# Kernel optimization log

Hardware: AMD Instinct MI355X
Metric: run time of the kernel (lower is better)

Reference implementation:

```python
import jax, jax.numpy as jnp
import numpy as np

NUM_HEADS = 16
ROPE_THETA = 10000.0


def apply_rope(x, positions):
    # x: [B, H, S, D], positions: [S] int
    d = x.shape[-1]
    inv_freq = ROPE_THETA ** (-jnp.arange(0, d, 2, dtype=jnp.float32) / d)  # [D/2]
    ang = positions.astype(jnp.float32)[:, None] * inv_freq[None, :]        # [S, D/2]
    cos, sin = jnp.cos(ang), jnp.sin(ang)                                   # [S, D/2]
    x1, x2 = x[..., 0::2], x[..., 1::2]                                     # even/odd pairs
    r1 = x1 * cos - x2 * sin
    r2 = x1 * sin + x2 * cos
    return jnp.stack([r1, r2], axis=-1).reshape(x.shape)


def setup_inputs() -> dict:
    key = jax.random.key(0)
    k1, k2, k3 = jax.random.split(key, 3)
    B, S, D = 2, 2048, 2048
    x = jax.random.normal(k1, (B, S, D), dtype=jnp.float32)
    token_positions = jnp.arange(S, dtype=jnp.int64)
    w_qkv = jax.random.normal(k2, (D, 3 * D), dtype=jnp.float32) * (D ** -0.5)
    w_o = jax.random.normal(k3, (D, D), dtype=jnp.float32) * (D ** -0.5)
    return {"x": x, "token_positions": token_positions, "w_qkv": w_qkv, "w_o": w_o}


def reference(x, token_positions, w_qkv, w_o):
    B, S, D = x.shape
    H = NUM_HEADS
    hd = D // H
    qkv = x @ w_qkv                                   # [B, S, 3D]
    qkv = qkv.reshape(B, S, 3, H, hd)                 # split '(r h d)'
    q = jnp.transpose(qkv[:, :, 0], (0, 2, 1, 3))     # [B, H, S, hd]
    k = jnp.transpose(qkv[:, :, 1], (0, 2, 1, 3))
    v = jnp.transpose(qkv[:, :, 2], (0, 2, 1, 3))
    q = apply_rope(q, token_positions)
    k = apply_rope(k, token_positions)
    scale = 1.0 / jnp.sqrt(jnp.float32(hd))
    scores = jnp.einsum('bhqd,bhkd->bhqk', q, k) * scale  # [B, H, S, S]
    causal = jnp.tril(jnp.ones((S, S), dtype=bool))
    scores = jnp.where(causal[None, None], scores, jnp.float32(-1e30))
    attn = jax.nn.softmax(scores, axis=-1)
    a = jnp.einsum('bhqk,bhkd->bhqd', attn, v)            # [B, H, S, hd]
    a = jnp.transpose(a, (0, 2, 1, 3)).reshape(B, S, D)   # merge heads, h-major
    return a @ w_o
```

## Files before the change

kernel.cpp:

```cpp
#include <hip/hip_runtime.h>

#define SEQ  2048
#define DIM  2048
#define NH   16
#define HD   128
#define TDIM 6144
#define TT   4096

typedef float  f32x4  __attribute__((ext_vector_type(4)));
typedef __bf16 bf16x8 __attribute__((ext_vector_type(8)));

__device__ __forceinline__ unsigned short f2b(float f){
  union { float f; unsigned int u; } x; x.f = f;
  unsigned int r = x.u + 0x7FFFu + ((x.u >> 16) & 1u);
  return (unsigned short)(r >> 16);
}
__device__ __forceinline__ float b2f(unsigned short b){
  union { unsigned int u; float f; } x; x.u = ((unsigned int)b) << 16;
  return x.f;
}
__device__ __forceinline__ void gl_lds16(const void* g, void* l){
  __builtin_amdgcn_global_load_lds((const __attribute__((address_space(1))) unsigned int*)g,
                                   (__attribute__((address_space(3))) unsigned int*)l, 16, 0, 0);
}

__global__ __launch_bounds__(256) void k_prep(const float* __restrict__ x,
                                              unsigned short* __restrict__ xb,
                                              float2* __restrict__ tab){
  int bid = blockIdx.x;
  if (bid < 8192){
    int i = bid * 256 + threadIdx.x;
    float4 v = ((const float4*)x)[i];
    ushort4 o; o.x = f2b(v.x); o.y = f2b(v.y); o.z = f2b(v.z); o.w = f2b(v.w);
    ((ushort4*)xb)[i] = o;
  } else {
    int i = (bid - 8192) * 256 + threadIdx.x;
    int s = i >> 6, f = i & 63;
    double inv = pow(10000.0, -2.0 * (double)f / 128.0);
    double a = (double)s * inv;
    tab[i] = make_float2((float)cos(a), (float)sin(a));
  }
}

__global__ __launch_bounds__(256) void k_tconvB(const float* __restrict__ w_qkv,
                                                unsigned short* __restrict__ wqkvT,
                                                const float* __restrict__ w_o,
                                                unsigned short* __restrict__ woT){
  const float* in; unsigned short* out; int C;
  if (blockIdx.z == 0){ in = w_qkv; out = wqkvT; C = TDIM; }
  else                { in = w_o;   out = woT;   C = DIM;  }
  int c0 = blockIdx.x * 32;
  if (c0 >= C) return;
  __shared__ float t[64][33];
  int r0 = blockIdx.y * 64;
  int tx = threadIdx.x & 31, ty = threadIdx.x >> 5;
  for (int i = 0; i < 8; i++)
    t[ty + i*8][tx] = in[(size_t)(r0 + ty + i*8) * C + c0 + tx];
  __syncthreads();
  for (int i = 0; i < 4; i++){
    int c = ty + i*8;
    ushort2 o2; o2.x = f2b(t[2*tx][c]); o2.y = f2b(t[2*tx+1][c]);
    *(ushort2*)&out[(size_t)(c0 + c) * DIM + r0 + 2*tx] = o2;
  }
}

__global__ __launch_bounds__(256) void k_rope(unsigned short* __restrict__ qkv,
                                              const float2* __restrict__ tab){
  int i = blockIdx.x * 256 + threadIdx.x;
  int t   = i >> 11;
  int rem = i & 2047;
  int p   = rem >> 10;
  int pi  = rem & 1023;
  int h   = pi >> 6;
  int f   = pi & 63;
  int s   = t & (SEQ - 1);
  size_t base = (size_t)t * TDIM + p * DIM + h * HD + f * 2;
  unsigned int v = *(const unsigned int*)&qkv[base];
  float x1 = b2f((unsigned short)(v & 0xffffu));
  float x2 = b2f((unsigned short)(v >> 16));
  float2 cs = tab[s * 64 + f];
  float sc2 = (p == 0) ? 0.08838834764831845f : 1.0f;
  float r1 = (x1 * cs.x - x2 * cs.y) * sc2;
  float r2 = (x1 * cs.y + x2 * cs.x) * sc2;
  *(unsigned int*)&qkv[base] = (unsigned int)f2b(r1) | ((unsigned int)f2b(r2) << 16);
}

__global__ __launch_bounds__(256) void k_tv(const unsigned short* __restrict__ qkv,
                                            unsigned short* __restrict__ vT){
  __shared__ unsigned short t[64][65];
  int bh = blockIdx.z; int b = bh >> 4, h = bh & 15;
  const unsigned short* V = qkv + (size_t)b * SEQ * TDIM + 2 * DIM + h * HD;
  unsigned short* o = vT + (size_t)bh * HD * SEQ;
  int s0 = blockIdx.x * 64, d0 = blockIdx.y * 64;
  int tx = threadIdx.x & 31, ty = threadIdx.x >> 5;
  for (int i = 0; i < 8; i++){
    unsigned int v = *(const unsigned int*)&V[(size_t)(s0 + ty + i*8) * TDIM + d0 + 2*tx];
    t[ty + i*8][2*tx]   = (unsigned short)(v & 0xffffu);
    t[ty + i*8][2*tx+1] = (unsigned short)(v >> 16);
  }
  __syncthreads();
  for (int i = 0; i < 8; i++){
    int d = ty + i*8;
    ushort2 o2; o2.x = t[2*tx][d]; o2.y = t[2*tx+1][d];
    *(ushort2*)&o[(size_t)(d0 + d) * SEQ + s0 + 2*tx] = o2;
  }
}

template<bool OUT_F32>
__global__ __launch_bounds__(512, 2) void k_gemm2(const unsigned short* __restrict__ A,
                                                  const unsigned short* __restrict__ BT,
                                                  void* __restrict__ Cout,
                                                  int M, int N, int K){
  __shared__ unsigned short sA[2*2*8192];
  __shared__ unsigned short sB[2*2*8192];
  int tid = threadIdx.x;
  int w = tid >> 6, l = tid & 63;
  int lm = l & 15, lq = l >> 4;
  int wm = w >> 2, wn = w & 3;
  int m0 = blockIdx.y * 256, n0 = blockIdx.x * 256;
  int NT = K >> 6;

  auto stA = [&](int buf, int half, int u){
    unsigned short* dst = sA + (buf*2 + half) * 8192;
    int grow0 = m0 + half*128;
#pragma unroll
    for (int j2 = 0; j2 < 2; j2++){
      int g = j2*512 + tid;
      int r = g >> 3, gc = g & 7;
      gl_lds16(A + (size_t)(grow0 + r) * K + u*64 + ((gc ^ (r & 7)) * 8), dst + g*8);
    }
  };
  auto stB = [&](int buf, int half, int u){
    unsigned short* dst = sB + (buf*2 + half) * 8192;
    int grow0 = n0 + half*128;
#pragma unroll
    for (int j2 = 0; j2 < 2; j2++){
      int g = j2*512 + tid;
      int r = g >> 3, gc = g & 7;
      gl_lds16(BT + (size_t)(grow0 + r) * K + u*64 + ((gc ^ (r & 7)) * 8), dst + g*8);
    }
  };

  f32x4 acc[2][2][4][2] = {};

  stA(0, 0, 0); stB(0, 1, 0); stA(0, 1, 0); stB(0, 0, 0);
  stA(1, 0, 1); stB(1, 1, 1);
  asm volatile("s_waitcnt vmcnt(4)" ::: "memory");
  __builtin_amdgcn_s_barrier();

  for (int t = 0; t < NT; t++){
    int cur = t & 1, nb = cur ^ 1;
    const unsigned short* sAb = sA + cur * 16384;
    const unsigned short* sBb = sB + cur * 16384;
    bf16x8 a[4][2], b0[2][2], b1[2][2];

#pragma unroll
    for (int i = 0; i < 4; i++){
      int r = wm*64 + i*16 + lm;
#pragma unroll
      for (int s = 0; s < 2; s++)
        a[i][s] = *(const bf16x8*)&sAb[r*64 + (((s*4 + lq) ^ (r & 7)) * 8)];
    }
#pragma unroll
    for (int j = 0; j < 2; j++){
      int r = wn*32 + j*16 + lm;
#pragma unroll
      for (int s = 0; s < 2; s++)
        b0[j][s] = *(const bf16x8*)&sBb[r*64 + (((s*4 + lq) ^ (r & 7)) * 8)];
    }
    __builtin_amdgcn_sched_barrier(0);
#pragma unroll
    for (int j = 0; j < 2; j++){
      int r = wn*32 + j*16 + lm;
#pragma unroll
      for (int s = 0; s < 2; s++)
        b1[j][s] = *(const bf16x8*)&sBb[8192 + r*64 + (((s*4 + lq) ^ (r & 7)) * 8)];
    }
    if (t + 1 < NT) stA(nb, 1, t + 1);
    asm volatile("s_waitcnt lgkmcnt(4)" ::: "memory");
    __builtin_amdgcn_sched_barrier(0);
    __builtin_amdgcn_s_setprio(1);
#pragma unroll
    for (int s = 0; s < 2; s++)
#pragma unroll
      for (int i = 0; i < 4; i++)
#pragma unroll
        for (int j = 0; j < 2; j++)
          acc[0][0][i][j] = __builtin_amdgcn_mfma_f32_16x16x32_bf16(a[i][s], b0[j][s],
                                                                    acc[0][0][i][j], 0, 0, 0);
    __builtin_amdgcn_s_setprio(0);
    __builtin_amdgcn_s_barrier();

    if (t + 1 < NT) stB(nb, 0, t + 1);
    asm volatile("s_waitcnt lgkmcnt(0)" ::: "memory");
    __builtin_amdgcn_sched_barrier(0);
    __builtin_amdgcn_s_setprio(1);
#pragma unroll
    for (int s = 0; s < 2; s++)
#pragma unroll
      for (int i = 0; i < 4; i++)
#pragma unroll
        for (int j = 0; j < 2; j++)
          acc[0][1][i][j] = __builtin_amdgcn_mfma_f32_16x16x32_bf16(a[i][s], b1[j][s],
                                                                    acc[0][1][i][j], 0, 0, 0);
    __builtin_amdgcn_s_setprio(0);
    __builtin_amdgcn_sched_barrier(0);
#pragma unroll
    for (int i = 0; i < 4; i++){
      int r = wm*64 + i*16 + lm;
#pragma unroll
      for (int s = 0; s < 2; s++)
        a[i][s] = *(const bf16x8*)&sAb[8192 + r*64 + (((s*4 + lq) ^ (r & 7)) * 8)];
    }
    __builtin_amdgcn_s_barrier();

    if (t + 2 < NT) stA(cur, 0, t + 2);
    asm volatile("s_waitcnt lgkmcnt(0)" ::: "memory");
    __builtin_amdgcn_sched_barrier(0);
    __builtin_amdgcn_s_setprio(1);
#pragma unroll
    for (int s = 0; s < 2; s++)
#pragma unroll
      for (int i = 0; i < 4; i++)
#pragma unroll
        for (int j = 0; j < 2; j++)
          acc[1][1][i][j] = __builtin_amdgcn_mfma_f32_16x16x32_bf16(a[i][s], b1[j][s],
                                                                    acc[1][1][i][j], 0, 0, 0);
    __builtin_amdgcn_s_setprio(0);
    __builtin_amdgcn_s_barrier();

    if (t + 2 < NT) stB(cur, 1, t + 2);
    __builtin_amdgcn_s_setprio(1);
#pragma unroll
    for (int s = 0; s < 2; s++)
#pragma unroll
      for (int i = 0; i < 4; i++)
#pragma unroll
        for (int j = 0; j < 2; j++)
          acc[1][0][i][j] = __builtin_amdgcn_mfma_f32_16x16x32_bf16(a[i][s], b0[j][s],
                                                                    acc[1][0][i][j], 0, 0, 0);
    __builtin_amdgcn_s_setprio(0);
    if (t + 2 < NT) asm volatile("s_waitcnt vmcnt(4)" ::: "memory");
    else            asm volatile("s_waitcnt vmcnt(0)" ::: "memory");
    __builtin_amdgcn_s_barrier();
  }

#pragma unroll
  for (int qm = 0; qm < 2; qm++)
#pragma unroll
    for (int qn = 0; qn < 2; qn++)
#pragma unroll
      for (int i = 0; i < 4; i++)
#pragma unroll
        for (int j = 0; j < 2; j++)
#pragma unroll
          for (int r = 0; r < 4; r++){
            int row = m0 + qm*128 + wm*64 + i*16 + lq*4 + r;
            int col = n0 + qn*128 + wn*32 + j*16 + lm;
            float v = acc[qm][qn][i][j][r];
            if (OUT_F32) ((float*)Cout)[(size_t)row * N + col] = v;
            else ((unsigned short*)Cout)[(size_t)row * N + col] = f2b(v);
          }
}

__global__ __launch_bounds__(512, 2) void k_gemm3(const unsigned short* __restrict__ A,
                                                  const unsigned short* __restrict__ BT,
                                                  float* __restrict__ Cout,
                                                  int M, int N, int K){
  __shared__ unsigned short sA[2*2*8192];
  __shared__ unsigned short sB[2*8192];
  int tid = threadIdx.x;
  int w = tid >> 6, l = tid & 63;
  int lm = l & 15, lq = l >> 4;
  int wm = w >> 2, wn = w & 3;
  int m0 = blockIdx.y * 256, n0 = blockIdx.x * 128;
  int NT = K >> 6;

  auto stA = [&](int buf, int half, int u){
    unsigned short* dst = sA + (buf*2 + half) * 8192;
    int grow0 = m0 + half*128;
#pragma unroll
    for (int j2 = 0; j2 < 2; j2++){
      int g = j2*512 + tid;
      int r = g >> 3, gc = g & 7;
      gl_lds16(A + (size_t)(grow0 + r) * K + u*64 + ((gc ^ (r & 7)) * 8), dst + g*8);
    }
  };
  auto stB = [&](int buf, int u){
    unsigned short* dst = sB + buf * 8192;
#pragma unroll
    for (int j2 = 0; j2 < 2; j2++){
      int g = j2*512 + tid;
      int r = g >> 3, gc = g & 7;
      gl_lds16(BT + (size_t)(n0 + r) * K + u*64 + ((gc ^ (r & 7)) * 8), dst + g*8);
    }
  };

  f32x4 acc[2][4][2] = {};

  stB(0, 0); stA(0, 0, 0); stA(0, 1, 0);
  asm volatile("s_waitcnt vmcnt(2)" ::: "memory");
  __builtin_amdgcn_s_barrier();

  for (int t = 0; t < NT; t++){
    int cur = t & 1, nb = cur ^ 1;
    const unsigned short* sAb = sA + cur * 16384;
    const unsigned short* sBb = sB + cur * 8192;
    bf16x8 a[4][2], b[2][2];

#pragma unroll
    for (int i = 0; i < 4; i++){
      int r = wm*64 + i*16 + lm;
#pragma unroll
      for (int s = 0; s < 2; s++)
        a[i][s] = *(const bf16x8*)&sAb[r*64 + (((s*4 + lq) ^ (r & 7)) * 8)];
    }
#pragma unroll
    for (int j = 0; j < 2; j++){
      int r = wn*32 + j*16 + lm;
#pragma unroll
      for (int s = 0; s < 2; s++)
        b[j][s] = *(const bf16x8*)&sBb[r*64 + (((s*4 + lq) ^ (r & 7)) * 8)];
    }
    if (t + 1 < NT){ stB(nb, t + 1); stA(nb, 0, t + 1); }
    asm volatile("s_waitcnt lgkmcnt(0)" ::: "memory");
    __builtin_amdgcn_sched_barrier(0);
    __builtin_amdgcn_s_setprio(1);
#pragma unroll
    for (int s = 0; s < 2; s++)
#pragma unroll
      for (int i = 0; i < 4; i++)
#pragma unroll
        for (int j = 0; j < 2; j++)
          acc[0][i][j] = __builtin_amdgcn_mfma_f32_16x16x32_bf16(a[i][s], b[j][s],
                                                                 acc[0][i][j], 0, 0, 0);
    __builtin_amdgcn_s_setprio(0);
    if (t + 1 < NT) asm volatile("s_waitcnt vmcnt(4)" ::: "memory");
    else            asm volatile("s_waitcnt vmcnt(0)" ::: "memory");
    __builtin_amdgcn_s_barrier();

#pragma unroll
    for (int i = 0; i < 4; i++){
      int r = wm*64 + i*16 + lm;
#pragma unroll
      for (int s = 0; s < 2; s++)
        a[i][s] = *(const bf16x8*)&sAb[8192 + r*64 + (((s*4 + lq) ^ (r & 7)) * 8)];
    }
    if (t + 1 < NT) stA(nb, 1, t + 1);
    asm volatile("s_waitcnt lgkmcnt(0)" ::: "memory");
    __builtin_amdgcn_sched_barrier(0);
    __builtin_amdgcn_s_setprio(1);
#pragma unroll
    for (int s = 0; s < 2; s++)
#pragma unroll
      for (int i = 0; i < 4; i++)
#pragma unroll
        for (int j = 0; j < 2; j++)
          acc[1][i][j] = __builtin_amdgcn_mfma_f32_16x16x32_bf16(a[i][s], b[j][s],
                                                                 acc[1][i][j], 0, 0, 0);
    __builtin_amdgcn_s_setprio(0);
    if (t + 1 < NT) asm volatile("s_waitcnt vmcnt(2)" ::: "memory");
    else            asm volatile("s_waitcnt vmcnt(0)" ::: "memory");
    __builtin_amdgcn_s_barrier();
  }

#pragma unroll
  for (int qm = 0; qm < 2; qm++)
#pragma unroll
    for (int i = 0; i < 4; i++)
#pragma unroll
      for (int j = 0; j < 2; j++)
#pragma unroll
        for (int r = 0; r < 4; r++){
          int row = m0 + qm*128 + wm*64 + i*16 + lq*4 + r;
          int col = n0 + wn*32 + j*16 + lm;
          Cout[(size_t)row * N + col] = acc[qm][i][j][r];
        }
}

__global__ __launch_bounds__(256, 1) void k_flash(const unsigned short* __restrict__ qkv,
                                                  const unsigned short* __restrict__ vT,
                                                  unsigned short* __restrict__ ab){
  __shared__ unsigned short sK[2][64*128];
  __shared__ unsigned short sV[2][128*64];
  __shared__ unsigned short sP[8][16][68];
  int bh = blockIdx.x; int b = bh >> 4, h = bh & 15;
  int pr = blockIdx.y;
  int tid = threadIdx.x; int w = tid >> 6, l = tid & 63;
  int lm = l & 15, lq = l >> 4;
  const unsigned short* Q  = qkv + (size_t)b * SEQ * TDIM + h * HD;
  const unsigned short* Kp = Q + DIM;
  const unsigned short* Vh = vT + (size_t)bh * HD * SEQ;

  auto stageK = [&](unsigned short* dst, int k0){
#pragma unroll
    for (int p = 0; p < 4; p++){
      int r = w*16 + p*4 + (l >> 4);
      int g = (l & 15) ^ (r & 15);
      gl_lds16(Kp + (size_t)(k0 + r) * TDIM + g*8, dst + (w*16 + p*4)*128 + l*8);
    }
  };
  auto stageV = [&](unsigned short* dst, int k0){
#pragma unroll
    for (int p = 0; p < 4; p++){
      int r = w*32 + p*8 + (l >> 3);
      int g = (l & 7) ^ (r & 7);
      gl_lds16(Vh + (size_t)r * SEQ + k0 + g*8, dst + (w*32 + p*8)*64 + l*8);
    }
  };

  for (int seg = 0; seg < 2; seg++){
    int qt = seg ? (15 - pr) : pr;
    int q0 = qt * 128;
    int nkt = 2*qt + 2;

    bf16x8 qf[2][4];
#pragma unroll
    for (int rg = 0; rg < 2; rg++)
#pragma unroll
      for (int ks = 0; ks < 4; ks++)
        qf[rg][ks] = *(const bf16x8*)&Q[(size_t)(q0 + w*32 + rg*16 + lm) * TDIM + ks*32 + lq*8];

    f32x4 o[2][8] = {};
    float l_i[2][4] = {};

    stageK(sK[0], 0);
    stageV(sV[0], 0);
    __syncthreads();

    for (int kt = 0; kt < nkt; kt++){
      int cur = kt & 1;
      if (kt + 1 < nkt){
        stageK(sK[cur ^ 1], (kt+1) * 64);
        stageV(sV[cur ^ 1], (kt+1) * 64);
      }
      const unsigned short* sKb = sK[cur];
      const unsigned short* sVb = sV[cur];

      f32x4 sc[2][4] = {};
#pragma unroll
      for (int ks = 0; ks < 4; ks++)
#pragma unroll
        for (int nt = 0; nt < 4; nt++){
          bf16x8 kf = *(const bf16x8*)&sKb[(nt*16 + lm)*128 + (((ks*4 + lq) ^ lm) * 8)];
          sc[0][nt] = __builtin_amdgcn_mfma_f32_16x16x32_bf16(qf[0][ks], kf, sc[0][nt], 0, 0, 0);
          sc[1][nt] = __builtin_amdgcn_mfma_f32_16x16x32_bf16(qf[1][ks], kf, sc[1][nt], 0, 0, 0);
        }

      int k0 = kt * 64;
      if (kt >= 2*qt){
#pragma unroll
        for (int rg = 0; rg < 2; rg++)
#pragma unroll
          for (int nt = 0; nt < 4; nt++)
#pragma unroll
            for (int r = 0; r < 4; r++){
              float e = __expf(sc[rg][nt][r]);
              if ((k0 + nt*16 + lm) > (q0 + w*32 + rg*16 + lq*4 + r)) e = 0.f;
              l_i[rg][r] += e;
              sP[w*2+rg][lq*4 + r][nt*16 + lm] = f2b(e);
            }
      } else {
#pragma unroll
        for (int rg = 0; rg < 2; rg++)
#pragma unroll
          for (int nt = 0; nt < 4; nt++)
#pragma unroll
            for (int r = 0; r < 4; r++){
              float e = __expf(sc[rg][nt][r]);
              l_i[rg][r] += e;
              sP[w*2+rg][lq*4 + r][nt*16 + lm] = f2b(e);
            }
      }

#pragma unroll
      for (int ks = 0; ks < 2; ks++){
        bf16x8 pf0 = *(const bf16x8*)&sP[w*2+0][lm][ks*32 + lq*8];
        bf16x8 pf1 = *(const bf16x8*)&sP[w*2+1][lm][ks*32 + lq*8];
#pragma unroll
        for (int nt = 0; nt < 8; nt++){
          bf16x8 vf = *(const bf16x8*)&sVb[(nt*16 + lm)*64 + (((ks*4 + lq) ^ (lm & 7)) * 8)];
          o[0][nt] = __builtin_amdgcn_mfma_f32_16x16x32_bf16(pf0, vf, o[0][nt], 0, 0, 0);
          o[1][nt] = __builtin_amdgcn_mfma_f32_16x16x32_bf16(pf1, vf, o[1][nt], 0, 0, 0);
        }
      }

      __syncthreads();
    }

#pragma unroll
    for (int rg = 0; rg < 2; rg++)
#pragma unroll
      for (int r = 0; r < 4; r++){
        float s = l_i[rg][r];
        for (int d = 1; d < 16; d <<= 1) s += __shfl_xor(s, d, 16);
        float inv = 1.0f / s;
        int trow = b * SEQ + q0 + w*32 + rg*16 + lq*4 + r;
#pragma unroll
        for (int nt = 0; nt < 8; nt++)
          ab[(size_t)trow * DIM + h * HD + nt*16 + lm] = f2b(o[rg][nt][r] * inv);
      }
  }
}

extern "C" void kernel_launch(void* const* d_in, const int* in_sizes, int n_in,
                              void* d_out, int out_size, void* d_ws, size_t ws_size,
                              hipStream_t stream){
  const float* x     = (const float*)d_in[0];
  const float* w_qkv = (const float*)d_in[2];
  const float* w_o   = (const float*)d_in[3];
  float* out = (float*)d_out;

  char* ws = (char*)d_ws;
  unsigned short* xb    = (unsigned short*)(ws);
  unsigned short* wqkvT = (unsigned short*)(ws + 16777216);
  unsigned short* woT   = (unsigned short*)(ws + 41943040);
  unsigned short* qkvb  = (unsigned short*)(ws + 50331648);
  unsigned short* vTb   = (unsigned short*)(ws + 100663296);
  unsigned short* abb   = (unsigned short*)(ws + 117440512);
  float2*         tab   = (float2*)(ws + 134217728);

  k_prep   <<<8704, 256, 0, stream>>>(x, xb, tab);
  k_tconvB <<<dim3(TDIM/32, DIM/64, 2), 256, 0, stream>>>(w_qkv, wqkvT, w_o, woT);
  k_gemm2<false><<<dim3(TDIM/256, TT/256), 512, 0, stream>>>(xb, wqkvT, qkvb, TT, TDIM, DIM);
  k_rope   <<<TT * 2048 / 256, 256, 0, stream>>>(qkvb, tab);
  k_tv     <<<dim3(SEQ/64, HD/64, 32), 256, 0, stream>>>(qkvb, vTb);
  k_flash  <<<dim3(32, 8), 256, 0, stream>>>(qkvb, vTb, abb);
  k_gemm3  <<<dim3(DIM/128, TT/256), 512, 0, stream>>>(abb, woT, out, TT, DIM, DIM);
}
```

Measured before the change: 385.3 us.

## Split flash attention work across 8 waves with 16 query rows each

Doubles the flash-attention block from 4 to 8 wavefronts, so each wave owns 16 query rows instead of 32. The K/V staging loads are redistributed across 512 threads and the per-wave register state (Q fragments, O accumulators, scores) is halved. The aim is more waves in flight per CU to hide latency in the 256-block grid. In exchange, each K/V fragment read from LDS now feeds one MFMA instead of two, and barriers must synchronise twice as many waves.

```diff
diff --git a/kernel.cpp b/kernel.cpp
--- a/kernel.cpp
+++ b/kernel.cpp
@@ -378,7 +378,7 @@
         }
 }
 
-__global__ __launch_bounds__(256, 1) void k_flash(const unsigned short* __restrict__ qkv,
+__global__ __launch_bounds__(512, 1) void k_flash(const unsigned short* __restrict__ qkv,
                                                   const unsigned short* __restrict__ vT,
                                                   unsigned short* __restrict__ ab){
   __shared__ unsigned short sK[2][64*128];
@@ -394,18 +394,18 @@
 
   auto stageK = [&](unsigned short* dst, int k0){
 #pragma unroll
-    for (int p = 0; p < 4; p++){
-      int r = w*16 + p*4 + (l >> 4);
-      int g = (l & 15) ^ (r & 15);
-      gl_lds16(Kp + (size_t)(k0 + r) * TDIM + g*8, dst + (w*16 + p*4)*128 + l*8);
+    for (int p = 0; p < 2; p++){
+      int g = p*512 + tid;
+      int r = g >> 4, gc = g & 15;
+      gl_lds16(Kp + (size_t)(k0 + r) * TDIM + ((gc ^ (r & 15)) * 8), dst + g*8);
     }
   };
   auto stageV = [&](unsigned short* dst, int k0){
 #pragma unroll
-    for (int p = 0; p < 4; p++){
-      int r = w*32 + p*8 + (l >> 3);
-      int g = (l & 7) ^ (r & 7);
-      gl_lds16(Vh + (size_t)r * SEQ + k0 + g*8, dst + (w*32 + p*8)*64 + l*8);
+    for (int p = 0; p < 2; p++){
+      int g = p*512 + tid;
+      int r = g >> 3, gc = g & 7;
+      gl_lds16(Vh + (size_t)r * SEQ + k0 + ((gc ^ (r & 7)) * 8), dst + g*8);
     }
   };
 
@@ -414,15 +414,14 @@
     int q0 = qt * 128;
     int nkt = 2*qt + 2;
 
-    bf16x8 qf[2][4];
-#pragma unroll
-    for (int rg = 0; rg < 2; rg++)
-#pragma unroll
-      for (int ks = 0; ks < 4; ks++)
-        qf[rg][ks] = *(const bf16x8*)&Q[(size_t)(q0 + w*32 + rg*16 + lm) * TDIM + ks*32 + lq*8];
-
-    f32x4 o[2][8] = {};
-    float l_i[2][4] = {};
+    int qrow = q0 + w*16 + lm;
+    bf16x8 qf[4];
+#pragma unroll
+    for (int ks = 0; ks < 4; ks++)
+      qf[ks] = *(const bf16x8*)&Q[(size_t)qrow * TDIM + ks*32 + lq*8];
+
+    f32x4 o[8] = {};
+    float l_i[4] = {0.f, 0.f, 0.f, 0.f};
 
     stageK(sK[0], 0);
     stageV(sV[0], 0);
@@ -437,51 +436,44 @@
       const unsigned short* sKb = sK[cur];
       const unsigned short* sVb = sV[cur];
 
-      f32x4 sc[2][4] = {};
+      f32x4 sc[4] = {};
 #pragma unroll
       for (int ks = 0; ks < 4; ks++)
 #pragma unroll
         for (int nt = 0; nt < 4; nt++){
           bf16x8 kf = *(const bf16x8*)&sKb[(nt*16 + lm)*128 + (((ks*4 + lq) ^ lm) * 8)];
-          sc[0][nt] = __builtin_amdgcn_mfma_f32_16x16x32_bf16(qf[0][ks], kf, sc[0][nt], 0, 0, 0);
-          sc[1][nt] = __builtin_amdgcn_mfma_f32_16x16x32_bf16(qf[1][ks], kf, sc[1][nt], 0, 0, 0);
+          sc[nt] = __builtin_amdgcn_mfma_f32_16x16x32_bf16(qf[ks], kf, sc[nt], 0, 0, 0);
         }
 
       int k0 = kt * 64;
       if (kt >= 2*qt){
 #pragma unroll
-        for (int rg = 0; rg < 2; rg++)
-#pragma unroll
-          for (int nt = 0; nt < 4; nt++)
-#pragma unroll
-            for (int r = 0; r < 4; r++){
-              float e = __expf(sc[rg][nt][r]);
-              if ((k0 + nt*16 + lm) > (q0 + w*32 + rg*16 + lq*4 + r)) e = 0.f;
-              l_i[rg][r] += e;
-              sP[w*2+rg][lq*4 + r][nt*16 + lm] = f2b(e);
-            }
+        for (int nt = 0; nt < 4; nt++)
+#pragma unroll
+          for (int r = 0; r < 4; r++){
+            float e = __expf(sc[nt][r]);
+            if ((k0 + nt*16 + lm) > (q0 + w*16 + lq*4 + r)) e = 0.f;
+            l_i[r] += e;
+            sP[w][lq*4 + r][nt*16 + lm] = f2b(e);
+          }
       } else {
 #pragma unroll
-        for (int rg = 0; rg < 2; rg++)
-#pragma unroll
-          for (int nt = 0; nt < 4; nt++)
-#pragma unroll
-            for (int r = 0; r < 4; r++){
-              float e = __expf(sc[rg][nt][r]);
-              l_i[rg][r] += e;
-              sP[w*2+rg][lq*4 + r][nt*16 + lm] = f2b(e);
-            }
+        for (int nt = 0; nt < 4; nt++)
+#pragma unroll
+          for (int r = 0; r < 4; r++){
+            float e = __expf(sc[nt][r]);
+            l_i[r] += e;
+            sP[w][lq*4 + r][nt*16 + lm] = f2b(e);
+          }
       }
 
 #pragma unroll
       for (int ks = 0; ks < 2; ks++){
-        bf16x8 pf0 = *(const bf16x8*)&sP[w*2+0][lm][ks*32 + lq*8];
-        bf16x8 pf1 = *(const bf16x8*)&sP[w*2+1][lm][ks*32 + lq*8];
+        bf16x8 pf = *(const bf16x8*)&sP[w][lm][ks*32 + lq*8];
 #pragma unroll
         for (int nt = 0; nt < 8; nt++){
           bf16x8 vf = *(const bf16x8*)&sVb[(nt*16 + lm)*64 + (((ks*4 + lq) ^ (lm & 7)) * 8)];
-          o[0][nt] = __builtin_amdgcn_mfma_f32_16x16x32_bf16(pf0, vf, o[0][nt], 0, 0, 0);
-          o[1][nt] = __builtin_amdgcn_mfma_f32_16x16x32_bf16(pf1, vf, o[1][nt], 0, 0, 0);
+          o[nt] = __builtin_amdgcn_mfma_f32_16x16x32_bf16(pf, vf, o[nt], 0, 0, 0);
         }
       }
 
@@ -489,17 +481,15 @@
     }
 
 #pragma unroll
-    for (int rg = 0; rg < 2; rg++)
-#pragma unroll
-      for (int r = 0; r < 4; r++){
-        float s = l_i[rg][r];
-        for (int d = 1; d < 16; d <<= 1) s += __shfl_xor(s, d, 16);
-        float inv = 1.0f / s;
-        int trow = b * SEQ + q0 + w*32 + rg*16 + lq*4 + r;
-#pragma unroll
-        for (int nt = 0; nt < 8; nt++)
-          ab[(size_t)trow * DIM + h * HD + nt*16 + lm] = f2b(o[rg][nt][r] * inv);
-      }
+    for (int r = 0; r < 4; r++){
+      float s = l_i[r];
+      for (int d = 1; d < 16; d <<= 1) s += __shfl_xor(s, d, 16);
+      float inv = 1.0f / s;
+      int trow = b * SEQ + q0 + w*16 + lq*4 + r;
+#pragma unroll
+      for (int nt = 0; nt < 8; nt++)
+        ab[(size_t)trow * DIM + h * HD + nt*16 + lm] = f2b(o[nt][r] * inv);
+    }
   }
 }
 
@@ -525,6 +515,6 @@
   k_gemm2<false><<<dim3(TDIM/256, TT/256), 512, 0, stream>>>(xb, wqkvT, qkvb, TT, TDIM, DIM);
   k_rope   <<<TT * 2048 / 256, 256, 0, stream>>>(qkvb, tab);
   k_tv     <<<dim3(SEQ/64, HD/64, 32), 256, 0, stream>>>(qkvb, vTb);
-  k_flash  <<<dim3(32, 8), 256, 0, stream>>>(qkvb, vTb, abb);
+  k_flash  <<<dim3(32, 8), 512, 0, stream>>>(qkvb, vTb, abb);
   k_gemm3  <<<dim3(DIM/128, TT/256), 512, 0, stream>>>(abb, woT, out, TT, DIM, DIM);
 }
```

Result: faster. 375.0 us (-2.7%).
